# Optimization experiments

Measured on AMD Instinct MI355X. Metric: run time of the kernel, lower is better.

Reference implementation:

```python
import jax, jax.numpy as jnp
import numpy as np

C = 256
NUM_HEADS = 8
GROUPS = C // 8
EPS = 1e-5


def conv1x1(x, w, b=None):
    # x: (B,C,H,W), w: (O,C)
    y = jnp.einsum('bchw,oc->bohw', x, w)
    if b is not None:
        y = y + b[None, :, None, None]
    return y


def dwconv3x3_s2(x, w):
    # depthwise 3x3, stride 2, padding 1; w: (C,1,3,3)
    return jax.lax.conv_general_dilated(
        x, w, window_strides=(2, 2), padding=((1, 1), (1, 1)),
        feature_group_count=x.shape[1],
        dimension_numbers=('NCHW', 'OIHW', 'NCHW'))


def group_norm(x, scale, bias, groups=GROUPS, eps=EPS):
    B, Cc, H, W = x.shape
    xg = x.reshape(B, groups, Cc // groups, H, W)
    mu = xg.mean(axis=(2, 3, 4), keepdims=True)
    var = xg.var(axis=(2, 3, 4), keepdims=True)
    xn = (xg - mu) * jax.lax.rsqrt(var + eps)
    return xn.reshape(B, Cc, H, W) * scale[None, :, None, None] + bias[None, :, None, None]


def silu(x):
    return x * jax.nn.sigmoid(x)


def downsample_branch(x, dw, gn1_s, gn1_b, pw, gn2_s, gn2_b):
    y = dwconv3x3_s2(x, dw)
    y = silu(group_norm(y, gn1_s, gn1_b))
    y = conv1x1(y, pw)
    y = silu(group_norm(y, gn2_s, gn2_b))
    return y


def setup_inputs() -> dict:
    key = jax.random.key(0)
    ks = jax.random.split(key, 20)
    s = 1.0 / np.sqrt(C)
    inp = {
        'x': jax.random.normal(ks[0], (32, C, 32, 32), dtype=jnp.float32),
        'wq': jax.random.normal(ks[1], (C, C), dtype=jnp.float32) * s,
        'bq': jnp.zeros((C,), jnp.float32),
        'wk': jax.random.normal(ks[2], (C, C), dtype=jnp.float32) * s,
        'bk': jnp.zeros((C,), jnp.float32),
        'wv': jax.random.normal(ks[3], (C, C), dtype=jnp.float32) * s,
        'bv': jnp.zeros((C,), jnp.float32),
        'k_dw': jax.random.normal(ks[4], (C, 1, 3, 3), dtype=jnp.float32) * (1.0 / 3.0),
        'k_gn1_s': jnp.ones((C,), jnp.float32), 'k_gn1_b': jnp.zeros((C,), jnp.float32),
        'k_pw': jax.random.normal(ks[5], (C, C), dtype=jnp.float32) * s,
        'k_gn2_s': jnp.ones((C,), jnp.float32), 'k_gn2_b': jnp.zeros((C,), jnp.float32),
        'v_dw': jax.random.normal(ks[6], (C, 1, 3, 3), dtype=jnp.float32) * (1.0 / 3.0),
        'v_gn1_s': jnp.ones((C,), jnp.float32), 'v_gn1_b': jnp.zeros((C,), jnp.float32),
        'v_pw': jax.random.normal(ks[7], (C, C), dtype=jnp.float32) * s,
        'v_gn2_s': jnp.ones((C,), jnp.float32), 'v_gn2_b': jnp.zeros((C,), jnp.float32),
    }
    return inp


def reference(x, wq, bq, wk, bk, wv, bv,
              k_dw, k_gn1_s, k_gn1_b, k_pw, k_gn2_s, k_gn2_b,
              v_dw, v_gn1_s, v_gn1_b, v_pw, v_gn2_s, v_gn2_b):
    B, Cc, H, W = x.shape
    nh = NUM_HEADS
    Dh = Cc // nh
    q = conv1x1(x, wq, bq)
    k = conv1x1(x, wk, bk)
    v = conv1x1(x, wv, bv)
    k = downsample_branch(k, k_dw, k_gn1_s, k_gn1_b, k_pw, k_gn2_s, k_gn2_b)
    v = downsample_branch(v, v_dw, v_gn1_s, v_gn1_b, v_pw, v_gn2_s, v_gn2_b)
    # view (B, nh, Dh, N) then transpose to (B, nh, N, Dh)
    qh = q.reshape(B, nh, Dh, -1).transpose(0, 1, 3, 2)
    kh = k.reshape(B, nh, Dh, -1).transpose(0, 1, 3, 2)
    vh = v.reshape(B, nh, Dh, -1).transpose(0, 1, 3, 2)
    scores = jnp.einsum('bhnd,bhmd->bhnm', qh, kh) / jnp.sqrt(jnp.float32(Dh))
    attn = jax.nn.softmax(scores, axis=-1)
    out = jnp.einsum('bhnm,bhmd->bhnd', attn, vh)  # (B,nh,N,Dh)
    out = out.transpose(0, 1, 3, 2).reshape(B, Cc, H, W)
    return out
```

## Files before the change

kernel.cpp:

```cpp
#include <hip/hip_runtime.h>
#include <cstddef>

#define B_  32
#define C_  256
#define N_  1024
#define M_  256
#define NH_ 8
#define DH_ 32

typedef __attribute__((ext_vector_type(4))) float f32x4;
typedef _Float16 half8h __attribute__((ext_vector_type(8)));
typedef _Float16 half4h __attribute__((ext_vector_type(4)));
typedef _Float16 half2h __attribute__((ext_vector_type(2)));

#define GLD16(g, l) __builtin_amdgcn_global_load_lds( \
    (const __attribute__((address_space(1))) unsigned int*)(g), \
    (__attribute__((address_space(3))) unsigned int*)(l), 16, 0, 0)

__global__ __launch_bounds__(256) void prep(
    const float* __restrict__ x,
    const float* __restrict__ w0, const float* __restrict__ w1,
    const float* __restrict__ w2, const float* __restrict__ w3,
    const float* __restrict__ w4,
    _Float16* __restrict__ xt, _Float16* __restrict__ wf5)
{
    const int bx = blockIdx.x;
    const int tid = threadIdx.x;

    if (bx < 2048) {
        __shared__ _Float16 tile[64][68];
        const int k0 = (bx & 3) * 64;
        const int n0 = ((bx >> 2) & 15) * 64;
        const int b  = bx >> 6;
        #pragma unroll
        for (int i = 0; i < 4; ++i) {
            const int kl = (tid >> 4) + i * 16;
            float4 v = *(const float4*)&x[((size_t)(b * C_) + k0 + kl) * N_ + n0 + (tid & 15) * 4];
            tile[(tid & 15) * 4 + 0][kl] = (_Float16)v.x;
            tile[(tid & 15) * 4 + 1][kl] = (_Float16)v.y;
            tile[(tid & 15) * 4 + 2][kl] = (_Float16)v.z;
            tile[(tid & 15) * 4 + 3][kl] = (_Float16)v.w;
        }
        __syncthreads();
        #pragma unroll
        for (int i = 0; i < 4; ++i) {
            const int nl = (tid >> 4) + i * 16;
            const int kl = (tid & 15) * 4;
            *(half4h*)&xt[((size_t)(b * N_) + n0 + nl) * C_ + k0 + kl] =
                *(const half4h*)&tile[nl][kl];
        }
    } else {
        const int wb = bx - 2048;
        const int which = wb >> 4;
        const int off0  = (wb & 15) * 4096;
        const float* src = which == 0 ? w0 : which == 1 ? w1 : which == 2 ? w2
                          : which == 3 ? w3 : w4;
        _Float16* dst = wf5 + (size_t)which * 65536 + off0;
        #pragma unroll
        for (int j = 0; j < 16; ++j)
            dst[tid + j * 256] = (_Float16)src[off0 + tid + j * 256];
    }
}

__global__ __launch_bounds__(256) void qkv_gemm(
    const _Float16* __restrict__ wf5, const _Float16* __restrict__ XT,
    const float* __restrict__ bq, const float* __restrict__ bk,
    const float* __restrict__ bv,
    _Float16* __restrict__ yq, _Float16* __restrict__ yk,
    _Float16* __restrict__ yv)
{
    __shared__ _Float16 Ah[128][64];
    __shared__ _Float16 Bh[128][64];

    const int flat    = blockIdx.x;
    const int logical = (flat & 7) * 192 + (flat >> 3);
    const int b       = logical / 48;
    const int r48     = logical % 48;
    const int which   = r48 >> 4;
    const int x       = r48 & 1;
    const int y       = (r48 >> 1) & 7;

    const _Float16* Wf = wf5 + (size_t)which * 65536;
    const float* bias = which == 0 ? bq : which == 1 ? bk : bv;
    _Float16* Y = which == 0 ? yq : which == 1 ? yk : yv;

    const int row0 = x * 128;
    const int n0   = y * 128;
    const int tid  = threadIdx.x;
    const int lane = tid & 63, w = tid >> 6;
    const int wm = (w >> 1) * 64, wn = (w & 1) * 64;
    const int l16 = lane & 15, lq = lane >> 4;

    const _Float16* XTb = XT + ((size_t)(b * N_) + n0) * C_;

    const int sr8 = lane >> 3;
    const int scs = ((lane & 7) ^ sr8) * 8;
    const _Float16* Ag = Wf  + (size_t)(row0 + w * 32 + sr8) * C_ + scs;
    const _Float16* Bg = XTb + (size_t)(w * 32 + sr8) * C_ + scs;

    f32x4 acc[4][4];
    #pragma unroll
    for (int i = 0; i < 4; ++i)
        #pragma unroll
        for (int j = 0; j < 4; ++j)
            #pragma unroll
            for (int r = 0; r < 4; ++r) acc[i][j][r] = 0.f;

    for (int k0 = 0; k0 < C_; k0 += 64) {
        __syncthreads();
        #pragma unroll
        for (int g = 0; g < 4; ++g) {
            GLD16(Ag + (size_t)(g * 8) * C_ + k0, &Ah[w * 32 + g * 8][0]);
            GLD16(Bg + (size_t)(g * 8) * C_ + k0, &Bh[w * 32 + g * 8][0]);
        }
        __syncthreads();

        #pragma unroll
        for (int kk = 0; kk < 2; ++kk) {
            half8h af[4], bf[4];
            #pragma unroll
            for (int t = 0; t < 4; ++t) {
                const int ra = wm + t * 16 + l16;
                af[t] = *(const half8h*)&Ah[ra][(((kk << 2) | lq) ^ (ra & 7)) * 8];
                const int rb = wn + t * 16 + l16;
                bf[t] = *(const half8h*)&Bh[rb][(((kk << 2) | lq) ^ (rb & 7)) * 8];
            }
            #pragma unroll
            for (int mt = 0; mt < 4; ++mt)
                #pragma unroll
                for (int nt = 0; nt < 4; ++nt)
                    acc[mt][nt] = __builtin_amdgcn_mfma_f32_16x16x32_f16(af[mt], bf[nt], acc[mt][nt], 0, 0, 0);
        }
    }

    if (which == 0) {
        const float qs = 0.17677669529663687f * 1.4426950408889634f;
        #pragma unroll
        for (int mt = 0; mt < 4; ++mt) {
            const int row = row0 + wm + mt * 16 + lq * 4;
            const float4 bv4 = *(const float4*)&bias[row];
            const int h  = row >> 5;
            const int d0 = row & 31;
            _Float16* yh = Y + ((size_t)(b * NH_) + h) * N_ * DH_ + d0;
            #pragma unroll
            for (int nt = 0; nt < 4; ++nt) {
                const int n = n0 + wn + nt * 16 + l16;
                half4h hv;
                hv[0] = (_Float16)((acc[mt][nt][0] + bv4.x) * qs);
                hv[1] = (_Float16)((acc[mt][nt][1] + bv4.y) * qs);
                hv[2] = (_Float16)((acc[mt][nt][2] + bv4.z) * qs);
                hv[3] = (_Float16)((acc[mt][nt][3] + bv4.w) * qs);
                *(half4h*)&yh[(size_t)n * DH_] = hv;
            }
        }
    } else {
        #pragma unroll
        for (int mt = 0; mt < 4; ++mt) {
            #pragma unroll
            for (int r = 0; r < 4; ++r) {
                const int row = row0 + wm + mt * 16 + lq * 4 + r;
                const float bv_ = bias[row];
                #pragma unroll
                for (int nt = 0; nt < 4; ++nt)
                    Y[((size_t)(b * C_) + row) * N_ + n0 + wn + nt * 16 + l16] =
                        (_Float16)(acc[mt][nt][r] + bv_);
            }
        }
    }
}

__global__ __launch_bounds__(256) void dw_gn(
    const _Float16* __restrict__ kin, const _Float16* __restrict__ vin,
    const float* __restrict__ kdw, const float* __restrict__ vdw,
    const float* __restrict__ kg1s, const float* __restrict__ kg1b,
    const float* __restrict__ vg1s, const float* __restrict__ vg1b,
    _Float16* __restrict__ kdT, _Float16* __restrict__ vdT)
{
    __shared__ _Float16 Xs[8192];
    __shared__ float red[8];
    const int bx = blockIdx.x;
    const int branch = bx >> 10;
    const int b = (bx >> 5) & 31;
    const int g = bx & 31;
    const _Float16* in = branch ? vin : kin;
    const float* dw = branch ? vdw : kdw;
    const float* gs = branch ? vg1s : kg1s;
    const float* gb = branch ? vg1b : kg1b;
    _Float16* outT = branch ? vdT : kdT;

    const int tid = threadIdx.x;

    {
        const _Float16* src = in + ((size_t)(b * C_) + g * 8) * 1024;
        #pragma unroll
        for (int i = 0; i < 4; ++i)
            *(half8h*)&Xs[tid * 8 + i * 2048] =
                *(const half8h*)&src[tid * 8 + i * 2048];
    }
    __syncthreads();

    const int oy = tid >> 4, ox = tid & 15;
    const int iy0 = oy*2 - 1;
    const int oxm = ox ? ox - 1 : 0;

    float vals[8];
    float s1 = 0.f, s2 = 0.f;
    #pragma unroll
    for (int cc = 0; cc < 8; ++cc) {
        const half2h* ip2 = (const half2h*)&Xs[cc * 1024];
        const float* wp = dw + (g*8 + cc)*9;
        float s = 0.f;
        #pragma unroll
        for (int dy = 0; dy < 3; ++dy) {
            const int iy = iy0 + dy;
            if (iy < 0 || iy > 31) continue;
            const int base = iy * 16;
            half2h A = ip2[base + oxm];
            half2h B = ip2[base + ox];
            const float t0 = ox ? (float)A[1] : 0.f;
            s += t0 * wp[dy*3 + 0]
               + (float)B[0] * wp[dy*3 + 1]
               + (float)B[1] * wp[dy*3 + 2];
        }
        vals[cc] = s;
        s1 += s; s2 += s*s;
    }
    #pragma unroll
    for (int off = 32; off > 0; off >>= 1) {
        s1 += __shfl_down(s1, off);
        s2 += __shfl_down(s2, off);
    }
    const int lane = tid & 63, wid = tid >> 6;
    if (lane == 0) { red[wid] = s1; red[4 + wid] = s2; }
    __syncthreads();
    s1 = red[0] + red[1] + red[2] + red[3];
    s2 = red[4] + red[5] + red[6] + red[7];
    const float mean = s1 * (1.f/2048.f);
    const float var  = s2 * (1.f/2048.f) - mean*mean;
    const float rstd = rsqrtf(var + 1e-5f);

    half8h o;
    #pragma unroll
    for (int cc = 0; cc < 8; ++cc) {
        const int c = g*8 + cc;
        const float xn = (vals[cc] - mean) * rstd * gs[c] + gb[c];
        o[cc] = (_Float16)(xn / (1.f + __expf(-xn)));
    }
    *(half8h*)&outT[((size_t)(b * M_) + tid) * C_ + g * 8] = o;
}

__global__ __launch_bounds__(256) void pw_gn2(
    const _Float16* __restrict__ wf5,
    const _Float16* __restrict__ kdT, const _Float16* __restrict__ vdT,
    const float* __restrict__ kg2s, const float* __restrict__ kg2b,
    const float* __restrict__ vg2s, const float* __restrict__ vg2b,
    _Float16* __restrict__ k2, _Float16* __restrict__ v2)
{
    __shared__ _Float16 Wlds[32][264];
    __shared__ _Float16 Bs[256][64];
    __shared__ float gmean[4], grstd[4];

    const int flat    = blockIdx.x;
    const int logical = (flat & 7) * 64 + (flat >> 3);
    const int xx      = logical & 7;
    const int b       = (logical >> 3) & 31;
    const int branch  = logical >> 8;

    const int ch0 = xx * 32;
    const _Float16* Wsrc = wf5 + (size_t)(3 + branch) * 65536;
    const _Float16* inT = branch ? vdT : kdT;
    const float* gs = branch ? vg2s : kg2s;
    const float* gb = branch ? vg2b : kg2b;
    _Float16* outp = branch ? v2 : k2;

    const int tid = threadIdx.x;
    const int lane = tid & 63, w = tid >> 6;
    const int l16 = lane & 15, quad = lane >> 4;

    {
        const int row = tid >> 3;
        const int off = (tid & 7) * 32;
        #pragma unroll
        for (int j = 0; j < 4; ++j)
            *(int4*)&Wlds[row][off + j * 8] =
                *(const int4*)&Wsrc[(size_t)(ch0 + row) * C_ + off + j * 8];
    }

    f32x4 acc[2][4];
    #pragma unroll
    for (int i = 0; i < 2; ++i)
        #pragma unroll
        for (int j = 0; j < 4; ++j)
            #pragma unroll
            for (int r = 0; r < 4; ++r) acc[i][j][r] = 0.f;

    const _Float16* inb = inT + (size_t)(b * M_) * C_;
    const int sr8 = lane >> 3;
    const int scs = ((lane & 7) ^ sr8) * 8;
    const _Float16* Bg = inb + (size_t)(w * 64 + sr8) * C_ + scs;

    for (int k0 = 0; k0 < C_; k0 += 64) {
        __syncthreads();
        #pragma unroll
        for (int g = 0; g < 8; ++g)
            GLD16(Bg + (size_t)(g * 8) * C_ + k0, &Bs[w * 64 + g * 8][0]);
        __syncthreads();

        #pragma unroll
        for (int kk = 0; kk < 2; ++kk) {
            half8h af[2], bf[4];
            #pragma unroll
            for (int mt = 0; mt < 2; ++mt)
                af[mt] = *(const half8h*)&Wlds[mt * 16 + l16][k0 + kk * 32 + quad * 8];
            #pragma unroll
            for (int nt = 0; nt < 4; ++nt) {
                const int rb = w * 64 + nt * 16 + l16;
                bf[nt] = *(const half8h*)&Bs[rb][(((kk << 2) | quad) ^ (rb & 7)) * 8];
            }
            #pragma unroll
            for (int mt = 0; mt < 2; ++mt)
                #pragma unroll
                for (int nt = 0; nt < 4; ++nt)
                    acc[mt][nt] = __builtin_amdgcn_mfma_f32_16x16x32_f16(af[mt], bf[nt], acc[mt][nt], 0, 0, 0);
        }
    }

    __syncthreads();
    _Float16 (*Rs)[264] = Wlds;
    #pragma unroll
    for (int mt = 0; mt < 2; ++mt)
        #pragma unroll
        for (int nt = 0; nt < 4; ++nt)
            #pragma unroll
            for (int r = 0; r < 4; ++r)
                Rs[mt * 16 + quad * 4 + r][w * 64 + nt * 16 + l16] = (_Float16)acc[mt][nt][r];
    __syncthreads();

    {
        float s1 = 0.f, s2 = 0.f;
        #pragma unroll
        for (int r = 0; r < 8; ++r)
            #pragma unroll
            for (int j = 0; j < 4; ++j) {
                const float vv = (float)Rs[w * 8 + r][lane * 4 + j];
                s1 += vv; s2 += vv * vv;
            }
        #pragma unroll
        for (int off = 32; off > 0; off >>= 1) {
            s1 += __shfl_xor(s1, off);
            s2 += __shfl_xor(s2, off);
        }
        if (lane == 0) {
            const float mean = s1 * (1.f / 2048.f);
            const float var  = s2 * (1.f / 2048.f) - mean * mean;
            gmean[w] = mean;
            grstd[w] = rsqrtf(var + 1e-5f);
        }
    }
    __syncthreads();

    #pragma unroll
    for (int cc = 0; cc < 32; ++cc) {
        const int g = cc >> 3;
        const float xn = ((float)Rs[cc][tid] - gmean[g]) * grstd[g] * gs[ch0 + cc] + gb[ch0 + cc];
        const float y  = xn / (1.f + __expf(-xn));
        outp[((size_t)(b * C_) + ch0 + cc) * M_ + tid] = (_Float16)y;
    }
}

__global__ __launch_bounds__(512) void attention_mfma(
    const _Float16* __restrict__ qT, const _Float16* __restrict__ k,
    const _Float16* __restrict__ v, float* __restrict__ out)
{
    __shared__ _Float16 Kl[256][40];
    __shared__ _Float16 VT[32][264];
    __shared__ float Os[8][32][36];

    const int bh = blockIdx.y;
    const int b = bh >> 3, h = bh & 7;
    const int n0 = blockIdx.x * 512;
    const int tid = threadIdx.x;
    const int lane = tid & 63, w = tid >> 6;
    const int l16 = lane & 15, quad = lane >> 4;
    const float SHIFT = 8.0f * 1.4426950408889634f;
    const f32x4 initS = {-SHIFT, -SHIFT, -SHIFT, -SHIFT};

    const size_t kvbase = ((size_t)(b * C_) + h * DH_) * (size_t)M_;

    {
        const int d2 = (tid & 15) * 2;
        const int m0 = (tid >> 4) * 8;
        half8h ka = *(const half8h*)&k[kvbase + (size_t)d2 * M_ + m0];
        half8h kb = *(const half8h*)&k[kvbase + (size_t)(d2 + 1) * M_ + m0];
        #pragma unroll
        for (int j = 0; j < 8; ++j) {
            union { _Float16 h[2]; unsigned u; } pk;
            pk.h[0] = ka[j]; pk.h[1] = kb[j];
            *(unsigned*)&Kl[m0 + j][d2] = pk.u;
        }
        const int vd  = tid & 31;
        const int vm0 = (tid >> 5) * 16;
        #pragma unroll
        for (int i = 0; i < 2; ++i)
            *(half8h*)&VT[vd][vm0 + i * 8] =
                *(const half8h*)&v[kvbase + (size_t)vd * M_ + vm0 + i * 8];
    }

    __syncthreads();

    #pragma unroll
    for (int qt2 = 0; qt2 < 2; ++qt2) {
        const int qn = n0 + qt2 * 256 + w * 32 + l16;
        const _Float16* qbase = qT + (((size_t)(b * NH_) + h) * N_ + qn) * DH_ + quad * 8;
        half8h qf[2];
        qf[0] = *(const half8h*)&qbase[0];
        qf[1] = *(const half8h*)&qbase[16 * DH_];

        f32x4 O[2][2];
        #pragma unroll
        for (int qt = 0; qt < 2; ++qt)
            #pragma unroll
            for (int dt = 0; dt < 2; ++dt)
                #pragma unroll
                for (int r = 0; r < 4; ++r) O[qt][dt][r] = 0.f;
        float lsum[2] = {0.f, 0.f};

        #pragma unroll
        for (int ch = 0; ch < 2; ++ch) {
            f32x4 S[2][8];
            __builtin_amdgcn_s_setprio(1);
            #pragma unroll
            for (int kt = 0; kt < 8; ++kt) {
                half8h kf = *(const half8h*)&Kl[ch * 128 + kt * 16 + l16][quad * 8];
                S[0][kt] = __builtin_amdgcn_mfma_f32_16x16x32_f16(kf, qf[0], initS, 0, 0, 0);
                S[1][kt] = __builtin_amdgcn_mfma_f32_16x16x32_f16(kf, qf[1], initS, 0, 0, 0);
            }
            __builtin_amdgcn_s_setprio(0);
            #pragma unroll
            for (int qt = 0; qt < 2; ++qt)
                #pragma unroll
                for (int kt = 0; kt < 8; ++kt)
                    #pragma unroll
                    for (int r = 0; r < 4; ++r) {
                        const float p = exp2f(S[qt][kt][r]);
                        S[qt][kt][r] = p;
                        lsum[qt] += p;
                    }
            __builtin_amdgcn_s_setprio(1);
            #pragma unroll
            for (int kt = 0; kt < 8; ++kt) {
                half4h vf[2];
                #pragma unroll
                for (int dt = 0; dt < 2; ++dt)
                    vf[dt] = *(const half4h*)&VT[dt * 16 + l16][ch * 128 + kt * 16 + quad * 4];
                #pragma unroll
                for (int qt = 0; qt < 2; ++qt) {
                    half2h p01 = __builtin_bit_cast(half2h,
                        __builtin_amdgcn_cvt_pkrtz(S[qt][kt][0], S[qt][kt][1]));
                    half2h p23 = __builtin_bit_cast(half2h,
                        __builtin_amdgcn_cvt_pkrtz(S[qt][kt][2], S[qt][kt][3]));
                    half4h pf = __builtin_shufflevector(p01, p23, 0, 1, 2, 3);
                    #pragma unroll
                    for (int dt = 0; dt < 2; ++dt)
                        O[qt][dt] = __builtin_amdgcn_mfma_f32_16x16x16f16(vf[dt], pf, O[qt][dt], 0, 0, 0);
                }
            }
            __builtin_amdgcn_s_setprio(0);
        }

        #pragma unroll
        for (int qt = 0; qt < 2; ++qt) {
            float ls = lsum[qt];
            ls += __shfl_xor(ls, 16);
            ls += __shfl_xor(ls, 32);
            const float inv = 1.f / ls;
            #pragma unroll
            for (int dt = 0; dt < 2; ++dt)
                #pragma unroll
                for (int r = 0; r < 4; ++r)
                    Os[w][dt * 16 + quad * 4 + r][qt * 16 + l16] = O[qt][dt][r] * inv;
        }
        const int qn0 = n0 + qt2 * 256 + w * 32;
        #pragma unroll
        for (int j = 0; j < 4; ++j) {
            const int row = j * 8 + (lane >> 3);
            const int col = (lane & 7) * 4;
            float4 vv = *(const float4*)&Os[w][row][col];
            *(float4*)&out[((size_t)(b * C_) + h * DH_ + row) * N_ + qn0 + col] = vv;
        }
    }
}

extern "C" void kernel_launch(void* const* d_in, const int* in_sizes, int n_in,
                              void* d_out, int out_size, void* d_ws, size_t ws_size,
                              hipStream_t stream)
{
    const float* x    = (const float*)d_in[0];
    const float* wq   = (const float*)d_in[1];
    const float* bq   = (const float*)d_in[2];
    const float* wk   = (const float*)d_in[3];
    const float* bk   = (const float*)d_in[4];
    const float* wv   = (const float*)d_in[5];
    const float* bv   = (const float*)d_in[6];
    const float* kdw  = (const float*)d_in[7];
    const float* kg1s = (const float*)d_in[8];
    const float* kg1b = (const float*)d_in[9];
    const float* kpw  = (const float*)d_in[10];
    const float* kg2s = (const float*)d_in[11];
    const float* kg2b = (const float*)d_in[12];
    const float* vdw  = (const float*)d_in[13];
    const float* vg1s = (const float*)d_in[14];
    const float* vg1b = (const float*)d_in[15];
    const float* vpw  = (const float*)d_in[16];
    const float* vg2s = (const float*)d_in[17];
    const float* vg2b = (const float*)d_in[18];
    float* out = (float*)d_out;

    const size_t HCN = (size_t)B_ * C_ * N_;
    const size_t HCM = (size_t)B_ * C_ * M_;
    _Float16* qh  = (_Float16*)d_ws;
    _Float16* k0h = qh  + HCN;
    _Float16* v0h = k0h + HCN;
    _Float16* XT  = v0h + HCN;
    _Float16* Wf5 = XT  + HCN;
    _Float16* kdT = Wf5 + 5 * 65536;
    _Float16* vdT = kdT + HCM;
    _Float16* k2  = vdT + HCM;
    _Float16* v2  = k2  + HCM;

    dim3 blk(256);

    prep<<<dim3(2128), blk, 0, stream>>>(x, wq, wk, wv, kpw, vpw, XT, Wf5);
    qkv_gemm<<<dim3(1536), blk, 0, stream>>>(Wf5, XT, bq, bk, bv, qh, k0h, v0h);
    dw_gn<<<dim3(2048), blk, 0, stream>>>(k0h, v0h, kdw, vdw,
                                          kg1s, kg1b, vg1s, vg1b, kdT, vdT);
    pw_gn2<<<dim3(512), blk, 0, stream>>>(Wf5, kdT, vdT,
                                          kg2s, kg2b, vg2s, vg2b, k2, v2);
    attention_mfma<<<dim3(2, B_ * NH_), dim3(512), 0, stream>>>(qh, k2, v2, out);
}
```

Before: 188.3 us.

## Fuse x transpose and fp16 conversion into the QKV GEMM B-tile load

The separate prep pass that transposed x to an fp16 N-major buffer (XT) is removed. The QKV GEMM now reads fp32 x directly, converts it with packed round-toward-zero conversion, and writes it transposed and swizzled into a larger 128x128 LDS B tile. The K loop is restructured into two halves, with the A tile reloaded in between. This saves the write and re-read of the intermediate buffer and one kernel's worth of work. In exchange, each GEMM block reads fp32 x (twice the bytes, repeated across the six blocks sharing a tile). The loads are plain register loads rather than async LDS loads, LDS use per block grows, and rounding changes from nearest to toward-zero.

```diff
diff --git a/kernel.cpp b/kernel.cpp
--- a/kernel.cpp
+++ b/kernel.cpp
@@ -18,85 +18,59 @@
     (__attribute__((address_space(3))) unsigned int*)(l), 16, 0, 0)
 
 __global__ __launch_bounds__(256) void prep(
-    const float* __restrict__ x,
     const float* __restrict__ w0, const float* __restrict__ w1,
     const float* __restrict__ w2, const float* __restrict__ w3,
     const float* __restrict__ w4,
-    _Float16* __restrict__ xt, _Float16* __restrict__ wf5)
+    _Float16* __restrict__ wf5)
 {
-    const int bx = blockIdx.x;
+    const int wb  = blockIdx.x;
     const int tid = threadIdx.x;
-
-    if (bx < 2048) {
-        __shared__ _Float16 tile[64][68];
-        const int k0 = (bx & 3) * 64;
-        const int n0 = ((bx >> 2) & 15) * 64;
-        const int b  = bx >> 6;
-        #pragma unroll
-        for (int i = 0; i < 4; ++i) {
-            const int kl = (tid >> 4) + i * 16;
-            float4 v = *(const float4*)&x[((size_t)(b * C_) + k0 + kl) * N_ + n0 + (tid & 15) * 4];
-            tile[(tid & 15) * 4 + 0][kl] = (_Float16)v.x;
-            tile[(tid & 15) * 4 + 1][kl] = (_Float16)v.y;
-            tile[(tid & 15) * 4 + 2][kl] = (_Float16)v.z;
-            tile[(tid & 15) * 4 + 3][kl] = (_Float16)v.w;
-        }
-        __syncthreads();
-        #pragma unroll
-        for (int i = 0; i < 4; ++i) {
-            const int nl = (tid >> 4) + i * 16;
-            const int kl = (tid & 15) * 4;
-            *(half4h*)&xt[((size_t)(b * N_) + n0 + nl) * C_ + k0 + kl] =
-                *(const half4h*)&tile[nl][kl];
-        }
-    } else {
-        const int wb = bx - 2048;
-        const int which = wb >> 4;
-        const int off0  = (wb & 15) * 4096;
-        const float* src = which == 0 ? w0 : which == 1 ? w1 : which == 2 ? w2
-                          : which == 3 ? w3 : w4;
-        _Float16* dst = wf5 + (size_t)which * 65536 + off0;
-        #pragma unroll
-        for (int j = 0; j < 16; ++j)
-            dst[tid + j * 256] = (_Float16)src[off0 + tid + j * 256];
-    }
+    const int which = wb >> 4;
+    const int off0  = (wb & 15) * 4096;
+    const float* src = which == 0 ? w0 : which == 1 ? w1 : which == 2 ? w2
+                      : which == 3 ? w3 : w4;
+    _Float16* dst = wf5 + (size_t)which * 65536 + off0;
+    #pragma unroll
+    for (int j = 0; j < 16; ++j)
+        dst[tid + j * 256] = (_Float16)src[off0 + tid + j * 256];
 }
 
 __global__ __launch_bounds__(256) void qkv_gemm(
-    const _Float16* __restrict__ wf5, const _Float16* __restrict__ XT,
+    const _Float16* __restrict__ wf5, const float* __restrict__ x,
     const float* __restrict__ bq, const float* __restrict__ bk,
     const float* __restrict__ bv,
     _Float16* __restrict__ yq, _Float16* __restrict__ yk,
     _Float16* __restrict__ yv)
 {
     __shared__ _Float16 Ah[128][64];
-    __shared__ _Float16 Bh[128][64];
+    __shared__ _Float16 Bh[128][128];
 
     const int flat    = blockIdx.x;
     const int logical = (flat & 7) * 192 + (flat >> 3);
     const int b       = logical / 48;
     const int r48     = logical % 48;
     const int which   = r48 >> 4;
-    const int x       = r48 & 1;
+    const int xt      = r48 & 1;
     const int y       = (r48 >> 1) & 7;
 
     const _Float16* Wf = wf5 + (size_t)which * 65536;
     const float* bias = which == 0 ? bq : which == 1 ? bk : bv;
     _Float16* Y = which == 0 ? yq : which == 1 ? yk : yv;
 
-    const int row0 = x * 128;
+    const int row0 = xt * 128;
     const int n0   = y * 128;
     const int tid  = threadIdx.x;
     const int lane = tid & 63, w = tid >> 6;
     const int wm = (w >> 1) * 64, wn = (w & 1) * 64;
     const int l16 = lane & 15, lq = lane >> 4;
 
-    const _Float16* XTb = XT + ((size_t)(b * N_) + n0) * C_;
-
     const int sr8 = lane >> 3;
     const int scs = ((lane & 7) ^ sr8) * 8;
-    const _Float16* Ag = Wf  + (size_t)(row0 + w * 32 + sr8) * C_ + scs;
-    const _Float16* Bg = XTb + (size_t)(w * 32 + sr8) * C_ + scs;
+    const _Float16* Ag = Wf + (size_t)(row0 + w * 32 + sr8) * C_ + scs;
+
+    const int tn  = tid & 127;
+    const int tk0 = (tid >> 7) * 64;
+    const float* xb = x + ((size_t)b * C_) * N_ + n0 + tn;
 
     f32x4 acc[4][4];
     #pragma unroll
@@ -106,30 +80,54 @@
             #pragma unroll
             for (int r = 0; r < 4; ++r) acc[i][j][r] = 0.f;
 
-    for (int k0 = 0; k0 < C_; k0 += 64) {
+    for (int half = 0; half < 2; ++half) {
+        const int kb = half * 128;
         __syncthreads();
         #pragma unroll
-        for (int g = 0; g < 4; ++g) {
-            GLD16(Ag + (size_t)(g * 8) * C_ + k0, &Ah[w * 32 + g * 8][0]);
-            GLD16(Bg + (size_t)(g * 8) * C_ + k0, &Bh[w * 32 + g * 8][0]);
+        for (int g = 0; g < 4; ++g)
+            GLD16(Ag + (size_t)(g * 8) * C_ + kb, &Ah[w * 32 + g * 8][0]);
+        #pragma unroll
+        for (int i = 0; i < 16; ++i) {
+            const int kq = tk0 + i * 4;
+            const float* xp = xb + (size_t)(kb + kq) * N_;
+            const float v0 = xp[0];
+            const float v1 = xp[N_];
+            const float v2 = xp[2 * N_];
+            const float v3 = xp[3 * N_];
+            half2h c01 = __builtin_bit_cast(half2h, __builtin_amdgcn_cvt_pkrtz(v0, v1));
+            half2h c23 = __builtin_bit_cast(half2h, __builtin_amdgcn_cvt_pkrtz(v2, v3));
+            half4h q4 = __builtin_shufflevector(c01, c23, 0, 1, 2, 3);
+            const int s = kq >> 3;
+            *(half4h*)&Bh[tn][(s ^ (tn & 7)) * 8 + (kq & 7)] = q4;
         }
         __syncthreads();
 
         #pragma unroll
-        for (int kk = 0; kk < 2; ++kk) {
-            half8h af[4], bf[4];
-            #pragma unroll
-            for (int t = 0; t < 4; ++t) {
-                const int ra = wm + t * 16 + l16;
-                af[t] = *(const half8h*)&Ah[ra][(((kk << 2) | lq) ^ (ra & 7)) * 8];
-                const int rb = wn + t * 16 + l16;
-                bf[t] = *(const half8h*)&Bh[rb][(((kk << 2) | lq) ^ (rb & 7)) * 8];
-            }
-            #pragma unroll
-            for (int mt = 0; mt < 4; ++mt)
-                #pragma unroll
-                for (int nt = 0; nt < 4; ++nt)
-                    acc[mt][nt] = __builtin_amdgcn_mfma_f32_16x16x32_f16(af[mt], bf[nt], acc[mt][nt], 0, 0, 0);
+        for (int kk2 = 0; kk2 < 2; ++kk2) {
+            if (kk2 == 1) {
+                __syncthreads();
+                #pragma unroll
+                for (int g = 0; g < 4; ++g)
+                    GLD16(Ag + (size_t)(g * 8) * C_ + kb + 64, &Ah[w * 32 + g * 8][0]);
+                __syncthreads();
+            }
+            #pragma unroll
+            for (int kkk = 0; kkk < 2; ++kkk) {
+                half8h af[4], bf[4];
+                #pragma unroll
+                for (int t = 0; t < 4; ++t) {
+                    const int ra = wm + t * 16 + l16;
+                    af[t] = *(const half8h*)&Ah[ra][(((kkk << 2) | lq) ^ (ra & 7)) * 8];
+                    const int rb = wn + t * 16 + l16;
+                    const int bs = kk2 * 8 + kkk * 4 + lq;
+                    bf[t] = *(const half8h*)&Bh[rb][(bs ^ (rb & 7)) * 8];
+                }
+                #pragma unroll
+                for (int mt = 0; mt < 4; ++mt)
+                    #pragma unroll
+                    for (int nt = 0; nt < 4; ++nt)
+                        acc[mt][nt] = __builtin_amdgcn_mfma_f32_16x16x32_f16(af[mt], bf[nt], acc[mt][nt], 0, 0, 0);
+            }
         }
     }
 
@@ -521,8 +519,7 @@
     _Float16* qh  = (_Float16*)d_ws;
     _Float16* k0h = qh  + HCN;
     _Float16* v0h = k0h + HCN;
-    _Float16* XT  = v0h + HCN;
-    _Float16* Wf5 = XT  + HCN;
+    _Float16* Wf5 = v0h + HCN;
     _Float16* kdT = Wf5 + 5 * 65536;
     _Float16* vdT = kdT + HCM;
     _Float16* k2  = vdT + HCM;
@@ -530,8 +527,8 @@
 
     dim3 blk(256);
 
-    prep<<<dim3(2128), blk, 0, stream>>>(x, wq, wk, wv, kpw, vpw, XT, Wf5);
-    qkv_gemm<<<dim3(1536), blk, 0, stream>>>(Wf5, XT, bq, bk, bv, qh, k0h, v0h);
+    prep<<<dim3(80), blk, 0, stream>>>(wq, wk, wv, kpw, vpw, Wf5);
+    qkv_gemm<<<dim3(1536), blk, 0, stream>>>(Wf5, x, bq, bk, bv, qh, k0h, v0h);
     dw_gn<<<dim3(2048), blk, 0, stream>>>(k0h, v0h, kdw, vdw,
                                           kg1s, kg1b, vg1s, vg1b, kdT, vdT);
     pw_gn2<<<dim3(512), blk, 0, stream>>>(Wf5, kdT, vdT,
```

Result: no change. 190.8 us (+1.4%).
